# Kernel optimization log

Hardware: AMD Instinct MI355X
Metric: run time of the kernel (lower is better)

The kernel has to match this reference:

```python
import jax, jax.numpy as jnp
import numpy as np

D_MODEL = 1024
NUM_HEADS = 16
D_K = D_MODEL // NUM_HEADS


def setup_inputs() -> dict:
    key = jax.random.key(0)
    ks = jax.random.split(key, 11)
    B, S, D = 4, 2048, D_MODEL
    scale = 1.0 / np.sqrt(D)
    return {
        "Q": jax.random.normal(ks[0], (B, S, D), jnp.float32),
        "K": jax.random.normal(ks[1], (B, S, D), jnp.float32),
        "V": jax.random.normal(ks[2], (B, S, D), jnp.float32),
        "Wq": jax.random.normal(ks[3], (D, D), jnp.float32) * scale,
        "bq": jnp.zeros((D,), jnp.float32),
        "Wk": jax.random.normal(ks[4], (D, D), jnp.float32) * scale,
        "bk": jnp.zeros((D,), jnp.float32),
        "Wv": jax.random.normal(ks[5], (D, D), jnp.float32) * scale,
        "bv": jnp.zeros((D,), jnp.float32),
        "Wo": jax.random.normal(ks[6], (D, D), jnp.float32) * scale,
        "bo": jnp.zeros((D,), jnp.float32),
    }


def reference(Q, K, V, Wq, bq, Wk, bk, Wv, bv, Wo, bo):
    B, S, D = Q.shape
    H, Dk = NUM_HEADS, D_K
    # projections: [B,S,D] -> [B,H,S,Dk]
    def proj(x, W, b):
        y = jnp.einsum('bsd,de->bse', x, W.T) + b  # torch Linear: x @ W.T + b
        return y.reshape(B, -1, H, Dk).transpose(0, 2, 1, 3)
    q = proj(Q, Wq, bq)
    k = proj(K, Wk, bk)
    v = proj(V, Wv, bv)
    scores = jnp.einsum('bhqd,bhkd->bhqk', q, k) / np.sqrt(Dk)  # [B,H,S,S]
    attn = jax.nn.softmax(scores, axis=-1)
    out = jnp.einsum('bhqk,bhkd->bhqd', attn, v)  # [B,H,S,Dk]
    out = out.transpose(0, 2, 1, 3).reshape(B, -1, D)
    return jnp.einsum('bsd,de->bse', out, Wo.T) + bo
```

## Files before the change

kernel.cpp:

```cpp
#include <hip/hip_runtime.h>


typedef __bf16 bhalf_t;
typedef __attribute__((ext_vector_type(8)))  __bf16 bf16x8;
typedef __attribute__((ext_vector_type(4)))  __bf16 bf16x4;
typedef __attribute__((ext_vector_type(4)))  float  f32x4;
typedef __attribute__((ext_vector_type(16))) float  f32x16;

typedef __attribute__((address_space(1))) void gvoid_t;
typedef __attribute__((address_space(3))) void lvoid_t;
#define GLD16(g, l) __builtin_amdgcn_global_load_lds((const gvoid_t*)(g), (lvoid_t*)(l), 16, 0, 0)

__global__ __launch_bounds__(256) void cvt_w(
    const float* __restrict__ Wq, const float* __restrict__ Wk,
    const float* __restrict__ Wv, const float* __restrict__ Wo,
    bhalf_t* __restrict__ Wqb, bhalf_t* __restrict__ Wkb,
    bhalf_t* __restrict__ Wvb, bhalf_t* __restrict__ Wob)
{
  size_t t = (size_t)blockIdx.x * 256 + threadIdx.x;
  int w = (int)(t >> 18); t &= 262143;
  const float* src = (w == 0) ? Wq  : (w == 1) ? Wk  : (w == 2) ? Wv  : Wo;
  bhalf_t*     dst = (w == 0) ? Wqb : (w == 1) ? Wkb : (w == 2) ? Wvb : Wob;
  float4 f = ((const float4*)src)[t];
  bf16x4 o;
  o.x = (bhalf_t)f.x; o.y = (bhalf_t)f.y; o.z = (bhalf_t)f.z; o.w = (bhalf_t)f.w;
  ((bf16x4*)dst)[t] = o;
}

__device__ __forceinline__ void gemm_core_128_swz(
    const bhalf_t* __restrict__ A, const bhalf_t* __restrict__ B,
    int bm, int bn, bhalf_t* As, bhalf_t* Bs, f32x4 acc[4][4])
{
  const int tid = threadIdx.x, lane = tid & 63, wave = tid >> 6;
  const int wm = wave >> 1, wn = wave & 1;
  const int quad = lane >> 4, tn = lane & 15;

  const int u    = (lane & 7) ^ (lane >> 3);
  const int roff = (lane >> 3) + 64 * (u >> 2);
  const int gk   = (u & 3) * 8;

  const bhalf_t* Ag0 = A + (size_t)(bm * 128 + wave * 8 + roff) * 1024 + gk;
  const bhalf_t* Ag1 = A + (size_t)(bm * 128 + (wave + 4) * 8 + roff) * 1024 + gk;
  const bhalf_t* Bg0 = B + (size_t)(bn * 128 + wave * 8 + roff) * 1024 + gk;
  const bhalf_t* Bg1 = B + (size_t)(bn * 128 + (wave + 4) * 8 + roff) * 1024 + gk;
  bhalf_t* Ad0 = As + wave * 512;  bhalf_t* Ad1 = As + (wave + 4) * 512;
  bhalf_t* Bd0 = Bs + wave * 512;  bhalf_t* Bd1 = Bs + (wave + 4) * 512;

  const int aswz = ((wm * 4 + quad) ^ (tn & 7)) * 8;
  const int bswz = ((wn * 4 + quad) ^ (tn & 7)) * 8;

  for (int k0 = 0; k0 < 1024; k0 += 32) {
    GLD16(Ag0 + k0, Ad0);
    GLD16(Ag1 + k0, Ad1);
    GLD16(Bg0 + k0, Bd0);
    GLD16(Bg1 + k0, Bd1);
    __syncthreads();
    bf16x8 af[4], bfr[4];
#pragma unroll
    for (int i = 0; i < 4; ++i)
      af[i] = *(const bf16x8*)(As + (i * 16 + tn) * 64 + aswz);
#pragma unroll
    for (int j = 0; j < 4; ++j)
      bfr[j] = *(const bf16x8*)(Bs + (j * 16 + tn) * 64 + bswz);
#pragma unroll
    for (int i = 0; i < 4; ++i)
#pragma unroll
      for (int j = 0; j < 4; ++j)
        acc[i][j] = __builtin_amdgcn_mfma_f32_16x16x32_bf16(af[i], bfr[j], acc[i][j], 0, 0, 0);
    __syncthreads();
  }
}

__global__ __launch_bounds__(256) void proj_gemm(
    const float* __restrict__ Qf, const float* __restrict__ Kf, const float* __restrict__ Vf,
    const bhalf_t* __restrict__ Wqb, const bhalf_t* __restrict__ Wkb, const bhalf_t* __restrict__ Wvb,
    const float* __restrict__ bq, const float* __restrict__ bk, const float* __restrict__ bv,
    bhalf_t* __restrict__ qo, bhalf_t* __restrict__ ko, bhalf_t* __restrict__ vto)
{
  __shared__ bhalf_t As[4096];
  __shared__ bhalf_t Bs[4096];
  const int seg = blockIdx.x >> 9;
  const int idx = blockIdx.x & 511;
  const int bm = idx & 63, bn = idx >> 6;

  const float *A; const bhalf_t *Bw; const float* bias; bhalf_t* out; float scale; int mode;
  if (seg == 0)      { A = Qf; Bw = Wqb; bias = bq; out = qo;  scale = 0.18033688f; mode = 0; }
  else if (seg == 1) { A = Kf; Bw = Wkb; bias = bk; out = ko;  scale = 1.0f;        mode = 0; }
  else               { A = Vf; Bw = Wvb; bias = bv; out = vto; scale = 1.0f;        mode = 1; }

  const int tid = threadIdx.x, lane = tid & 63, wave = tid >> 6;
  const int wm = wave >> 1, wn = wave & 1;
  const int quad = lane >> 4, tn = lane & 15;

  const int u    = (lane & 7) ^ (lane >> 3);
  const int roff = (lane >> 3) + 64 * (u >> 2);
  const int gk   = (u & 3) * 8;

  const float* Af0 = A + (size_t)(bm * 128 + wave * 8 + roff) * 1024 + gk;
  const float* Af1 = A + (size_t)(bm * 128 + (wave + 4) * 8 + roff) * 1024 + gk;
  bhalf_t* Ad0 = As + wave * 512 + lane * 8;
  bhalf_t* Ad1 = As + (wave + 4) * 512 + lane * 8;
  const bhalf_t* Bg0 = Bw + (size_t)(bn * 128 + wave * 8 + roff) * 1024 + gk;
  const bhalf_t* Bg1 = Bw + (size_t)(bn * 128 + (wave + 4) * 8 + roff) * 1024 + gk;
  bhalf_t* Bd0 = Bs + wave * 512;
  bhalf_t* Bd1 = Bs + (wave + 4) * 512;

  const int aswz = ((wm * 4 + quad) ^ (tn & 7)) * 8;
  const int bswz = ((wn * 4 + quad) ^ (tn & 7)) * 8;

  f32x4 acc[4][4];
#pragma unroll
  for (int i = 0; i < 4; ++i)
#pragma unroll
    for (int j = 0; j < 4; ++j)
      acc[i][j] = (f32x4){0.f, 0.f, 0.f, 0.f};

  for (int k0 = 0; k0 < 1024; k0 += 32) {
    GLD16(Bg0 + k0, Bd0);
    GLD16(Bg1 + k0, Bd1);
    float4 a00 = *(const float4*)(Af0 + k0);
    float4 a01 = *(const float4*)(Af0 + k0 + 4);
    float4 a10 = *(const float4*)(Af1 + k0);
    float4 a11 = *(const float4*)(Af1 + k0 + 4);
    bf16x8 v0, v1;
    v0[0] = (bhalf_t)a00.x; v0[1] = (bhalf_t)a00.y;
    v0[2] = (bhalf_t)a00.z; v0[3] = (bhalf_t)a00.w;
    v0[4] = (bhalf_t)a01.x; v0[5] = (bhalf_t)a01.y;
    v0[6] = (bhalf_t)a01.z; v0[7] = (bhalf_t)a01.w;
    v1[0] = (bhalf_t)a10.x; v1[1] = (bhalf_t)a10.y;
    v1[2] = (bhalf_t)a10.z; v1[3] = (bhalf_t)a10.w;
    v1[4] = (bhalf_t)a11.x; v1[5] = (bhalf_t)a11.y;
    v1[6] = (bhalf_t)a11.z; v1[7] = (bhalf_t)a11.w;
    *(bf16x8*)Ad0 = v0;
    *(bf16x8*)Ad1 = v1;
    __syncthreads();
    bf16x8 af[4], bfr[4];
#pragma unroll
    for (int i = 0; i < 4; ++i)
      af[i] = *(const bf16x8*)(As + (i * 16 + tn) * 64 + aswz);
#pragma unroll
    for (int j = 0; j < 4; ++j)
      bfr[j] = *(const bf16x8*)(Bs + (j * 16 + tn) * 64 + bswz);
#pragma unroll
    for (int i = 0; i < 4; ++i)
#pragma unroll
      for (int j = 0; j < 4; ++j)
        acc[i][j] = __builtin_amdgcn_mfma_f32_16x16x32_bf16(af[i], bfr[j], acc[i][j], 0, 0, 0);
    __syncthreads();
  }

#pragma unroll
  for (int i = 0; i < 4; ++i)
#pragma unroll
    for (int j = 0; j < 4; ++j) {
      const int n = bn * 128 + wn * 64 + j * 16 + tn;
      const float bsv = bias[n];
      const int h = n >> 6, dk = n & 63;
#pragma unroll
      for (int r = 0; r < 4; ++r) {
        const int m = bm * 128 + wm * 64 + i * 16 + quad * 4 + r;
        const int b = m >> 11, s = m & 2047;
        const float v = (acc[i][j][r] + bsv) * scale;
        size_t addr;
        if (mode == 0) addr = (((size_t)(b * 16 + h)) * 2048 + s) * 64 + dk;
        else {
          const int s2 = (s & ~12) | ((s & 4) << 1) | ((s & 8) >> 1);
          addr = (((size_t)(b * 16 + h)) * 64 + dk) * 2048 + s2;
        }
        out[addr] = (bhalf_t)v;
      }
    }
}

__global__ __launch_bounds__(256) void out_gemm(
    const bhalf_t* __restrict__ A, const bhalf_t* __restrict__ Bw,
    const float* __restrict__ bias, float* __restrict__ Cout)
{
  __shared__ bhalf_t As[4096];
  __shared__ bhalf_t Bs[4096];
  const int bm = blockIdx.x & 63, bn = blockIdx.x >> 6;

  f32x4 acc[4][4];
#pragma unroll
  for (int i = 0; i < 4; ++i)
#pragma unroll
    for (int j = 0; j < 4; ++j)
      acc[i][j] = (f32x4){0.f, 0.f, 0.f, 0.f};

  gemm_core_128_swz(A, Bw, bm, bn, As, Bs, acc);

  const int lane = threadIdx.x & 63, wave = threadIdx.x >> 6;
  const int wm = wave >> 1, wn = wave & 1, quad = lane >> 4, tn = lane & 15;
#pragma unroll
  for (int i = 0; i < 4; ++i)
#pragma unroll
    for (int j = 0; j < 4; ++j) {
      const int n = bn * 128 + wn * 64 + j * 16 + tn;
      const float bsv = bias[n];
#pragma unroll
      for (int r = 0; r < 4; ++r) {
        const int m = bm * 128 + wm * 64 + i * 16 + quad * 4 + r;
        Cout[(size_t)m * 1024 + n] = acc[i][j][r] + bsv;
      }
    }
}

__global__ __launch_bounds__(256, 2) void attn_kernel(
    const bhalf_t* __restrict__ qp, const bhalf_t* __restrict__ kp,
    const bhalf_t* __restrict__ vtp, bhalf_t* __restrict__ outp)
{
  __shared__ bhalf_t Klds[4096];
  __shared__ bhalf_t Vtlds[4096];

  const int tid = threadIdx.x, lane = tid & 63, wave = tid >> 6;
  const int q31 = lane & 31, h = lane >> 5;
  const int bh = blockIdx.y, qt = blockIdx.x;

  const bhalf_t* qbase = qp + (((size_t)bh * 2048) + qt * 256 + wave * 64 + q31) * 64;
  bf16x8 qf[2][4];
#pragma unroll
  for (int qs = 0; qs < 2; ++qs)
#pragma unroll
    for (int ks = 0; ks < 4; ++ks)
      qf[qs][ks] = *(const bf16x8*)(qbase + qs * 32 * 64 + ks * 16 + h * 8);

  f32x16 Ot[2][2];
#pragma unroll
  for (int qs = 0; qs < 2; ++qs)
#pragma unroll
    for (int dd = 0; dd < 2; ++dd)
#pragma unroll
      for (int i = 0; i < 16; ++i) Ot[qs][dd][i] = 0.f;
  float Lp[2] = {0.f, 0.f};

  const bhalf_t* kbase  = kp  + (size_t)bh * 2048 * 64;
  const bhalf_t* vtbase = vtp + (size_t)bh * 64 * 2048;

  const int rloc = lane >> 3;
  const int cg8  = ((lane & 7) ^ rloc) * 8;
  const int q7 = q31 & 7;

  for (int kv0 = 0; kv0 < 2048; kv0 += 64) {
#pragma unroll
    for (int i = 0; i < 2; ++i) {
      const int r0 = (wave * 2 + i) * 8;
      GLD16(kbase + (size_t)(kv0 + r0 + rloc) * 64 + cg8, Klds + r0 * 64);
      GLD16(vtbase + (size_t)(r0 + rloc) * 2048 + kv0 + cg8, Vtlds + r0 * 64);
    }
    __syncthreads();

    bf16x8 pb[2][4];
#pragma unroll
    for (int mb = 0; mb < 2; ++mb) {
      bf16x8 ka[4];
#pragma unroll
      for (int ks = 0; ks < 4; ++ks)
        ka[ks] = *(const bf16x8*)(Klds + (mb * 32 + q31) * 64 + ((2 * ks + h) ^ q7) * 8);
#pragma unroll
      for (int qs = 0; qs < 2; ++qs) {
        f32x16 S;
#pragma unroll
        for (int i = 0; i < 16; ++i) S[i] = 0.f;
#pragma unroll
        for (int ks = 0; ks < 4; ++ks)
          S = __builtin_amdgcn_mfma_f32_32x32x16_bf16(ka[ks], qf[qs][ks], S, 0, 0, 0);
        float ls = 0.f;
#pragma unroll
        for (int half = 0; half < 2; ++half) {
          bf16x8 pk;
#pragma unroll
          for (int j = 0; j < 8; ++j) {
            const float e = __builtin_amdgcn_exp2f(S[half * 8 + j]);
            ls += e;
            pk[j] = (bhalf_t)e;
          }
          pb[qs][mb * 2 + half] = pk;
        }
        Lp[qs] += ls;
      }
    }

#pragma unroll
    for (int dd = 0; dd < 2; ++dd)
#pragma unroll
      for (int kb = 0; kb < 4; ++kb) {
        const bf16x8 va = *(const bf16x8*)(Vtlds + (dd * 32 + q31) * 64 + ((2 * kb + h) ^ q7) * 8);
#pragma unroll
        for (int qs = 0; qs < 2; ++qs)
          Ot[qs][dd] = __builtin_amdgcn_mfma_f32_32x32x16_bf16(va, pb[qs][kb], Ot[qs][dd], 0, 0, 0);
      }
    __syncthreads();
  }

  const int b = bh >> 4, hh = bh & 15;
#pragma unroll
  for (int qs = 0; qs < 2; ++qs) {
    const float Lt = Lp[qs] + __shfl_xor(Lp[qs], 32, 64);
    const float linv = 1.0f / Lt;
    const int s = qt * 256 + wave * 64 + qs * 32 + q31;
    bhalf_t* ob = outp + ((size_t)(b * 2048 + s)) * 1024 + hh * 64;
#pragma unroll
    for (int dd = 0; dd < 2; ++dd)
#pragma unroll
      for (int g = 0; g < 4; ++g) {
        bf16x4 o;
        o.x = (bhalf_t)(Ot[qs][dd][4 * g + 0] * linv);
        o.y = (bhalf_t)(Ot[qs][dd][4 * g + 1] * linv);
        o.z = (bhalf_t)(Ot[qs][dd][4 * g + 2] * linv);
        o.w = (bhalf_t)(Ot[qs][dd][4 * g + 3] * linv);
        *(bf16x4*)(ob + dd * 32 + g * 8 + h * 4) = o;
      }
  }
}

extern "C" void kernel_launch(void* const* d_in, const int* in_sizes, int n_in,
                              void* d_out, int out_size, void* d_ws, size_t ws_size,
                              hipStream_t stream)
{
  const float* Q  = (const float*)d_in[0];
  const float* K  = (const float*)d_in[1];
  const float* V  = (const float*)d_in[2];
  const float* Wq = (const float*)d_in[3];
  const float* bq = (const float*)d_in[4];
  const float* Wk = (const float*)d_in[5];
  const float* bk = (const float*)d_in[6];
  const float* Wv = (const float*)d_in[7];
  const float* bv = (const float*)d_in[8];
  const float* Wo = (const float*)d_in[9];
  const float* bo = (const float*)d_in[10];

  char* ws = (char*)d_ws;
  const size_t SZ = 8192ull * 1024 * 2;
  const size_t WZ = 1024ull * 1024 * 2;
  bhalf_t* Wqb  = (bhalf_t*)(ws);
  bhalf_t* Wkb  = (bhalf_t*)(ws + WZ);
  bhalf_t* Wvb  = (bhalf_t*)(ws + 2 * WZ);
  bhalf_t* Wob  = (bhalf_t*)(ws + 3 * WZ);
  bhalf_t* q_p  = (bhalf_t*)(ws + 4 * WZ);
  bhalf_t* k_p  = (bhalf_t*)(ws + 4 * WZ + SZ);
  bhalf_t* vt_p = (bhalf_t*)(ws + 4 * WZ + 2 * SZ);
  bhalf_t* attn_o = (bhalf_t*)(ws + 4 * WZ + 3 * SZ);

  cvt_w<<<4096, 256, 0, stream>>>(Wq, Wk, Wv, Wo, Wqb, Wkb, Wvb, Wob);
  proj_gemm<<<1536, 256, 0, stream>>>(Q, K, V, Wqb, Wkb, Wvb,
                                      bq, bk, bv, q_p, k_p, vt_p);
  attn_kernel<<<dim3(8, 64), 256, 0, stream>>>(q_p, k_p, vt_p, attn_o);
  out_gemm<<<512, 256, 0, stream>>>(attn_o, Wob, bo, (float*)d_out);
}
```

Measured before the change: 356.2 us.

## Double-buffer K/V tiles in attention and load fp32 A tiles directly to LDS

The attention kernel now double-buffers its K and V^T tiles in shared memory and prefetches the next tile while the current one is being computed, so global load latency can overlap the MFMA work. The projection GEMM stops going through registers and converting fp32 activations to bf16 before the LDS store. It now streams the fp32 tile straight into LDS with global_load_lds and converts to bf16 when reading MFMA fragments. This doubles LDS use in both kernels, which may lower occupancy, and the conversion now runs on every fragment read. The attention loop also drops the barrier after its loads, so correctness relies on the trailing barrier and on how vmcnt waits are handled.

```diff
diff --git a/kernel.cpp b/kernel.cpp
--- a/kernel.cpp
+++ b/kernel.cpp
@@ -77,7 +77,7 @@
     const float* __restrict__ bq, const float* __restrict__ bk, const float* __restrict__ bv,
     bhalf_t* __restrict__ qo, bhalf_t* __restrict__ ko, bhalf_t* __restrict__ vto)
 {
-  __shared__ bhalf_t As[4096];
+  __shared__ float   Asf[4096];
   __shared__ bhalf_t Bs[4096];
   const int seg = blockIdx.x >> 9;
   const int idx = blockIdx.x & 511;
@@ -92,20 +92,23 @@
   const int wm = wave >> 1, wn = wave & 1;
   const int quad = lane >> 4, tn = lane & 15;
 
-  const int u    = (lane & 7) ^ (lane >> 3);
-  const int roff = (lane >> 3) + 64 * (u >> 2);
-  const int gk   = (u & 3) * 8;
-
-  const float* Af0 = A + (size_t)(bm * 128 + wave * 8 + roff) * 1024 + gk;
-  const float* Af1 = A + (size_t)(bm * 128 + (wave + 4) * 8 + roff) * 1024 + gk;
-  bhalf_t* Ad0 = As + wave * 512 + lane * 8;
-  bhalf_t* Ad1 = As + (wave + 4) * 512 + lane * 8;
-  const bhalf_t* Bg0 = Bw + (size_t)(bn * 128 + wave * 8 + roff) * 1024 + gk;
-  const bhalf_t* Bg1 = Bw + (size_t)(bn * 128 + (wave + 4) * 8 + roff) * 1024 + gk;
+  const int u = (lane & 7) ^ (lane >> 3);
+
+  const float* Ag[4];
+#pragma unroll
+  for (int i = 0; i < 4; ++i)
+    Ag[i] = A + (size_t)(bm * 128 + wave * 32 + i * 8 + (lane >> 3)) * 1024 + u * 4;
+
+  const int roffB = (lane >> 3) + 64 * (u >> 2);
+  const int gkB   = (u & 3) * 8;
+  const bhalf_t* Bg0 = Bw + (size_t)(bn * 128 + wave * 8 + roffB) * 1024 + gkB;
+  const bhalf_t* Bg1 = Bw + (size_t)(bn * 128 + (wave + 4) * 8 + roffB) * 1024 + gkB;
   bhalf_t* Bd0 = Bs + wave * 512;
   bhalf_t* Bd1 = Bs + (wave + 4) * 512;
 
-  const int aswz = ((wm * 4 + quad) ^ (tn & 7)) * 8;
+  const int arow = (wm * 64 + tn) * 32;
+  const int alo  = ((2 * quad)     ^ (tn & 7)) * 4;
+  const int ahi  = ((2 * quad + 1) ^ (tn & 7)) * 4;
   const int bswz = ((wn * 4 + quad) ^ (tn & 7)) * 8;
 
   f32x4 acc[4][4];
@@ -118,26 +121,22 @@
   for (int k0 = 0; k0 < 1024; k0 += 32) {
     GLD16(Bg0 + k0, Bd0);
     GLD16(Bg1 + k0, Bd1);
-    float4 a00 = *(const float4*)(Af0 + k0);
-    float4 a01 = *(const float4*)(Af0 + k0 + 4);
-    float4 a10 = *(const float4*)(Af1 + k0);
-    float4 a11 = *(const float4*)(Af1 + k0 + 4);
-    bf16x8 v0, v1;
-    v0[0] = (bhalf_t)a00.x; v0[1] = (bhalf_t)a00.y;
-    v0[2] = (bhalf_t)a00.z; v0[3] = (bhalf_t)a00.w;
-    v0[4] = (bhalf_t)a01.x; v0[5] = (bhalf_t)a01.y;
-    v0[6] = (bhalf_t)a01.z; v0[7] = (bhalf_t)a01.w;
-    v1[0] = (bhalf_t)a10.x; v1[1] = (bhalf_t)a10.y;
-    v1[2] = (bhalf_t)a10.z; v1[3] = (bhalf_t)a10.w;
-    v1[4] = (bhalf_t)a11.x; v1[5] = (bhalf_t)a11.y;
-    v1[6] = (bhalf_t)a11.z; v1[7] = (bhalf_t)a11.w;
-    *(bf16x8*)Ad0 = v0;
-    *(bf16x8*)Ad1 = v1;
+#pragma unroll
+    for (int i = 0; i < 4; ++i)
+      GLD16(Ag[i] + k0, Asf + (wave * 4 + i) * 256);
     __syncthreads();
     bf16x8 af[4], bfr[4];
 #pragma unroll
-    for (int i = 0; i < 4; ++i)
-      af[i] = *(const bf16x8*)(As + (i * 16 + tn) * 64 + aswz);
+    for (int i = 0; i < 4; ++i) {
+      const f32x4 lo = *(const f32x4*)(Asf + arow + i * 512 + alo);
+      const f32x4 hi = *(const f32x4*)(Asf + arow + i * 512 + ahi);
+      bf16x8 v;
+      v[0] = (bhalf_t)lo[0]; v[1] = (bhalf_t)lo[1];
+      v[2] = (bhalf_t)lo[2]; v[3] = (bhalf_t)lo[3];
+      v[4] = (bhalf_t)hi[0]; v[5] = (bhalf_t)hi[1];
+      v[6] = (bhalf_t)hi[2]; v[7] = (bhalf_t)hi[3];
+      af[i] = v;
+    }
 #pragma unroll
     for (int j = 0; j < 4; ++j)
       bfr[j] = *(const bf16x8*)(Bs + (j * 16 + tn) * 64 + bswz);
@@ -209,8 +208,8 @@
     const bhalf_t* __restrict__ qp, const bhalf_t* __restrict__ kp,
     const bhalf_t* __restrict__ vtp, bhalf_t* __restrict__ outp)
 {
-  __shared__ bhalf_t Klds[4096];
-  __shared__ bhalf_t Vtlds[4096];
+  __shared__ bhalf_t Klds[2][4096];
+  __shared__ bhalf_t Vtlds[2][4096];
 
   const int tid = threadIdx.x, lane = tid & 63, wave = tid >> 6;
   const int q31 = lane & 31, h = lane >> 5;
@@ -240,14 +239,26 @@
   const int cg8  = ((lane & 7) ^ rloc) * 8;
   const int q7 = q31 & 7;
 
+#pragma unroll
+  for (int i = 0; i < 2; ++i) {
+    const int r0 = (wave * 2 + i) * 8;
+    GLD16(kbase + (size_t)(r0 + rloc) * 64 + cg8, &Klds[0][r0 * 64]);
+    GLD16(vtbase + (size_t)(r0 + rloc) * 2048 + cg8, &Vtlds[0][r0 * 64]);
+  }
+  __syncthreads();
+
   for (int kv0 = 0; kv0 < 2048; kv0 += 64) {
-#pragma unroll
-    for (int i = 0; i < 2; ++i) {
-      const int r0 = (wave * 2 + i) * 8;
-      GLD16(kbase + (size_t)(kv0 + r0 + rloc) * 64 + cg8, Klds + r0 * 64);
-      GLD16(vtbase + (size_t)(r0 + rloc) * 2048 + kv0 + cg8, Vtlds + r0 * 64);
-    }
-    __syncthreads();
+    const int cur = (kv0 >> 6) & 1, nxt = cur ^ 1;
+    if (kv0 < 2048 - 64) {
+#pragma unroll
+      for (int i = 0; i < 2; ++i) {
+        const int r0 = (wave * 2 + i) * 8;
+        GLD16(kbase + (size_t)(kv0 + 64 + r0 + rloc) * 64 + cg8, &Klds[nxt][r0 * 64]);
+        GLD16(vtbase + (size_t)(r0 + rloc) * 2048 + (kv0 + 64) + cg8, &Vtlds[nxt][r0 * 64]);
+      }
+    }
+    const bhalf_t* Kc = Klds[cur];
+    const bhalf_t* Vc = Vtlds[cur];
 
     bf16x8 pb[2][4];
 #pragma unroll
@@ -255,7 +266,7 @@
       bf16x8 ka[4];
 #pragma unroll
       for (int ks = 0; ks < 4; ++ks)
-        ka[ks] = *(const bf16x8*)(Klds + (mb * 32 + q31) * 64 + ((2 * ks + h) ^ q7) * 8);
+        ka[ks] = *(const bf16x8*)(Kc + (mb * 32 + q31) * 64 + ((2 * ks + h) ^ q7) * 8);
 #pragma unroll
       for (int qs = 0; qs < 2; ++qs) {
         f32x16 S;
@@ -284,7 +295,7 @@
     for (int dd = 0; dd < 2; ++dd)
 #pragma unroll
       for (int kb = 0; kb < 4; ++kb) {
-        const bf16x8 va = *(const bf16x8*)(Vtlds + (dd * 32 + q31) * 64 + ((2 * kb + h) ^ q7) * 8);
+        const bf16x8 va = *(const bf16x8*)(Vc + (dd * 32 + q31) * 64 + ((2 * kb + h) ^ q7) * 8);
 #pragma unroll
         for (int qs = 0; qs < 2; ++qs)
           Ot[qs][dd] = __builtin_amdgcn_mfma_f32_32x32x16_bf16(va, pb[qs][kb], Ot[qs][dd], 0, 0, 0);
```

Result: no change. 350.1 us (-1.7%).
